# Optimization experiments

Measured on AMD Instinct MI355X. Metric: run time of the kernel, lower is better.

Reference implementation:

```python
import jax, jax.numpy as jnp
import numpy as np

D_MODEL = 256
D_STATE = 256
BATCH = 32
SEQ = 4096
RMIN, RMAX = 0.9, 0.999
NEG_SLOPE = 0.01
EPS = 1e-5


def layer_norm(x, w=None, b=None):
    m = jnp.mean(x, axis=-1, keepdims=True)
    v = jnp.var(x, axis=-1, keepdims=True)
    y = (x - m) * jax.lax.rsqrt(v + EPS)
    if w is not None:
        y = y * w + b
    return y


def leaky_relu(x):
    return jnp.where(x >= 0, x, NEG_SLOPE * x)


def setup_inputs() -> dict:
    key = jax.random.key(0)
    ks = jax.random.split(key, 12)
    x = jax.random.normal(ks[0], (BATCH, SEQ, D_MODEL), dtype=jnp.float32)
    # LRU ring init: |lambda| uniform in [rmin, rmax], phase uniform in [0, 2pi]
    u1 = jax.random.uniform(ks[1], (D_STATE,), dtype=jnp.float32)
    u2 = jax.random.uniform(ks[2], (D_STATE,), dtype=jnp.float32)
    nu_log = jnp.log(-0.5 * jnp.log(u1 * (RMAX**2 - RMIN**2) + RMIN**2))
    theta_log = jnp.log(2 * jnp.pi * u2)
    lam_mod = jnp.exp(-jnp.exp(nu_log))
    gamma_log = jnp.log(jnp.sqrt(1.0 - lam_mod**2))
    B_re = jax.random.normal(ks[3], (D_STATE, D_MODEL)) / np.sqrt(2 * D_MODEL)
    B_im = jax.random.normal(ks[4], (D_STATE, D_MODEL)) / np.sqrt(2 * D_MODEL)
    C_re = jax.random.normal(ks[5], (D_STATE, D_STATE)) / np.sqrt(D_STATE)
    C_im = jax.random.normal(ks[6], (D_STATE, D_STATE)) / np.sqrt(D_STATE)
    Dm = jax.random.normal(ks[7], (D_STATE, D_MODEL)) / np.sqrt(D_MODEL)
    Wl = jax.random.normal(ks[8], (D_MODEL, D_STATE)) / np.sqrt(D_STATE)
    bl = jax.random.normal(ks[9], (D_MODEL,)) * 0.02
    Wr = jax.random.normal(ks[10], (D_MODEL, D_STATE)) / np.sqrt(D_STATE)
    br = jax.random.normal(ks[11], (D_MODEL,)) * 0.02
    ones_m = jnp.ones((D_MODEL,), jnp.float32)
    zeros_m = jnp.zeros((D_MODEL,), jnp.float32)
    ones_s = jnp.ones((D_STATE,), jnp.float32)
    zeros_s = jnp.zeros((D_STATE,), jnp.float32)
    return {
        "x": x,
        "ln1_w": ones_m, "ln1_b": zeros_m,
        "nu_log": nu_log, "theta_log": theta_log, "gamma_log": gamma_log,
        "B_re": B_re, "B_im": B_im, "C_re": C_re, "C_im": C_im, "Dm": Dm,
        "ln2_w": ones_s, "ln2_b": zeros_s,
        "Wl": Wl, "bl": bl, "Wr": Wr, "br": br,
        "ln4_w": ones_m, "ln4_b": zeros_m,
    }


def reference(x, ln1_w, ln1_b, nu_log, theta_log, gamma_log, B_re, B_im,
              C_re, C_im, Dm, ln2_w, ln2_b, Wl, bl, Wr, br, ln4_w, ln4_b):
    # pre-norm + residual skip
    x1 = layer_norm(x, ln1_w, ln1_b)          # [B, T, d_model]
    skip = x1
    u = leaky_relu(x1)
    # LRU: h_t = lambda * h_{t-1} + gamma * (B u_t); y = Re(C h) + D u
    lam_mod = jnp.exp(-jnp.exp(nu_log))
    theta = jnp.exp(theta_log)
    lr = lam_mod * jnp.cos(theta)             # [N]
    li = lam_mod * jnp.sin(theta)
    gam = jnp.exp(gamma_log)
    bu_re = gam * jnp.einsum('btd,nd->btn', u, B_re)  # [B, T, N]
    bu_im = gam * jnp.einsum('btd,nd->btn', u, B_im)
    bu_re_t = jnp.swapaxes(bu_re, 0, 1)       # [T, B, N]
    bu_im_t = jnp.swapaxes(bu_im, 0, 1)

    def step(carry, inp):
        hr, hi = carry
        br_t, bi_t = inp
        hr2 = lr * hr - li * hi + br_t
        hi2 = lr * hi + li * hr + bi_t
        return (hr2, hi2), (hr2, hi2)

    h0 = (jnp.zeros((x.shape[0], lr.shape[0]), x.dtype),
          jnp.zeros((x.shape[0], lr.shape[0]), x.dtype))
    (hr_last, hi_last), (hr, hi) = jax.lax.scan(step, h0, (bu_re_t, bu_im_t))
    hr = jnp.swapaxes(hr, 0, 1)               # [B, T, N]
    hi = jnp.swapaxes(hi, 0, 1)
    y = (jnp.einsum('btn,mn->btm', hr, C_re)
         - jnp.einsum('btn,mn->btm', hi, C_im)
         + jnp.einsum('btd,md->btm', u, Dm))  # [B, T, d_state]
    # post-norm + nonlinearity
    y = leaky_relu(layer_norm(y, ln2_w, ln2_b))
    # gated bilinear MLP
    xl = layer_norm(y @ Wl.T + bl)            # no affine
    xr = layer_norm(y @ Wr.T + br)
    out = layer_norm(xl * xr, ln4_w, ln4_b) + skip
    return out
```

## Files before the change

### kernel.cpp

```cpp
#include <hip/hip_runtime.h>
#include <cstdint>
#include <cstddef>

#define DEV __device__ __forceinline__

typedef unsigned short u16;
typedef short short8 __attribute__((ext_vector_type(8)));
typedef float floatx4 __attribute__((ext_vector_type(4)));

constexpr int BB = 32;
constexpr int TT = 4096;
constexpr int RR = BB * TT;
constexpr int CH = 64;
constexpr int LC = TT / CH;

constexpr size_t OFF_LAM  = 0;
constexpr size_t OFF_LAML = 2048;
constexpr size_t OFF_GAM  = 4096;
constexpr size_t OFF_B1   = 8192;
constexpr size_t OFF_B2   = OFF_B1 + (size_t)512 * 256 * 2;
constexpr size_t OFF_B3   = OFF_B2 + (size_t)256 * 768 * 2;
constexpr size_t OFF_BIG  = 2ull << 20;
constexpr size_t SZB      = (size_t)RR * 256 * 2;

DEV float bf2f(u16 u) {
    unsigned int i = ((unsigned int)u) << 16;
    float f;
    __builtin_memcpy(&f, &i, 4);
    return f;
}
DEV u16 f2bf(float f) {
    unsigned int i;
    __builtin_memcpy(&i, &f, 4);
    i += 0x7fffu + ((i >> 16) & 1u);
    return (u16)(i >> 16);
}

DEV void gload16(const void* g, void* l) {
    __builtin_amdgcn_global_load_lds(
        (const __attribute__((address_space(1))) unsigned int*)g,
        (__attribute__((address_space(3))) unsigned int*)l, 16, 0, 0);
}
DEV void gload4(const void* g, void* l) {
    __builtin_amdgcn_global_load_lds(
        (const __attribute__((address_space(1))) unsigned int*)g,
        (__attribute__((address_space(3))) unsigned int*)l, 4, 0, 0);
}

__global__ __launch_bounds__(256)
void k_setup(const float* __restrict__ nu_log, const float* __restrict__ theta_log,
             const float* __restrict__ gamma_log,
             const float* __restrict__ B_re, const float* __restrict__ B_im,
             const float* __restrict__ C_re, const float* __restrict__ C_im,
             const float* __restrict__ Dm,
             const float* __restrict__ Wl, const float* __restrict__ Wr,
             char* __restrict__ ws)
{
    float2* lam  = (float2*)(ws + OFF_LAM);
    float2* lamL = (float2*)(ws + OFF_LAML);
    float*  gam  = (float*)(ws + OFF_GAM);
    u16* B1 = (u16*)(ws + OFF_B1);
    u16* B2 = (u16*)(ws + OFF_B2);
    u16* B3 = (u16*)(ws + OFF_B3);
    int g = blockIdx.x * 256 + threadIdx.x;
    int stride = gridDim.x * 256;
    if (g < 256) {
        float mod = expf(-expf(nu_log[g]));
        float th  = expf(theta_log[g]);
        float lr = mod * cosf(th), li = mod * sinf(th);
        lam[g] = make_float2(lr, li);
        gam[g] = expf(gamma_log[g]);
        float pr = 1.f, pi = 0.f;
        for (int i = 0; i < LC; i++) { float nr = pr*lr - pi*li; pi = pr*li + pi*lr; pr = nr; }
        lamL[g] = make_float2(pr, pi);
    }
    for (int i = g; i < 512*256; i += stride) {
        int n = i >> 8, d = i & 255;
        B1[i] = f2bf(n < 256 ? B_re[n*256 + d] : B_im[(n-256)*256 + d]);
    }
    for (int i = g; i < 256*768; i += stride) {
        int m = i / 768, k = i - m*768;
        float v = (k < 256) ? C_re[m*256 + k]
                : (k < 512) ? -C_im[m*256 + (k-256)]
                            : Dm[m*256 + (k-512)];
        B2[i] = f2bf(v);
    }
    for (int i = g; i < 512*256; i += stride) {
        int n = i >> 8, d = i & 255;
        B3[i] = f2bf(n < 256 ? Wl[n*256 + d] : Wr[(n-256)*256 + d]);
    }
}

__global__ __launch_bounds__(256)
void k_ln1(const float* __restrict__ x, const float* __restrict__ w, const float* __restrict__ b,
           u16* __restrict__ u, u16* __restrict__ skip)
{
    const int wv = threadIdx.x >> 6, lane = threadIdx.x & 63;
    const size_t row = (size_t)blockIdx.x * 4 + wv;
    float4 v = ((const float4*)(x + row * 256))[lane];
    float s = v.x + v.y + v.z + v.w;
    float q = v.x*v.x + v.y*v.y + v.z*v.z + v.w*v.w;
    #pragma unroll
    for (int o = 32; o; o >>= 1) { s += __shfl_xor(s, o); q += __shfl_xor(q, o); }
    const float m  = s * (1.f/256.f);
    const float rs = rsqrtf(q * (1.f/256.f) - m*m + 1e-5f);
    const float4 wv4 = ((const float4*)w)[lane];
    const float4 bv4 = ((const float4*)b)[lane];
    float y0 = (v.x - m) * rs * wv4.x + bv4.x;
    float y1 = (v.y - m) * rs * wv4.y + bv4.y;
    float y2 = (v.z - m) * rs * wv4.z + bv4.z;
    float y3 = (v.w - m) * rs * wv4.w + bv4.w;
    ((ushort4*)(skip + row * 256))[lane] = make_ushort4(f2bf(y0), f2bf(y1), f2bf(y2), f2bf(y3));
    float u0 = y0 >= 0.f ? y0 : 0.01f * y0;
    float u1 = y1 >= 0.f ? y1 : 0.01f * y1;
    float u2 = y2 >= 0.f ? y2 : 0.01f * y2;
    float u3 = y3 >= 0.f ? y3 : 0.01f * y3;
    ((ushort4*)(u + row * 256))[lane] = make_ushort4(f2bf(u0), f2bf(u1), f2bf(u2), f2bf(u3));
}

__global__ __launch_bounds__(256)
void k_gemm1(const u16* __restrict__ A0, const u16* __restrict__ Bmat,
             u16* __restrict__ O0, u16* __restrict__ O1, const float* __restrict__ p0)
{
    __shared__ alignas(16) u16 As[2][128 * 64];
    __shared__ alignas(16) u16 Bs[2][128 * 64];
    const int wid = threadIdx.x >> 6, lane = threadIdx.x & 63;
    const int rowbase = blockIdx.x * 128;
    const int ct = blockIdx.y;
    const u16* Bbase = Bmat + (size_t)ct * 128 * 256;
    const int srow  = lane >> 3;
    const int sslot = (lane & 7) ^ srow;
    floatx4 acc[4][4] = {};

    auto stage = [&](int kt, int pb) {
        int kofs = kt * 64;
        #pragma unroll
        for (int i = 0; i < 4; i++) {
            int grp = wid * 4 + i;
            int row = grp * 8 + srow;
            gload16(A0 + (size_t)(rowbase + row) * 256 + kofs + sslot * 8,
                    (char*)&As[pb][0] + grp * 1024);
            gload16(Bbase + (size_t)row * 256 + kofs + sslot * 8,
                    (char*)&Bs[pb][0] + grp * 1024);
        }
    };

    stage(0, 0);
    const int wm = wid >> 1, wn = wid & 1;
    for (int kt = 0; kt < 4; ++kt) {
        const int pb = kt & 1;
        if (kt + 1 < 4) {
            stage(kt + 1, pb ^ 1);
            asm volatile("s_waitcnt vmcnt(8)" ::: "memory");
        } else {
            asm volatile("s_waitcnt vmcnt(0)" ::: "memory");
        }
        __builtin_amdgcn_s_barrier();
        short8 af[2][4], bfr[2][4];
        #pragma unroll
        for (int kk = 0; kk < 2; kk++) {
            const int rslot = (kk * 4 + (lane >> 4)) ^ (lane & 7);
            #pragma unroll
            for (int mi = 0; mi < 4; mi++)
                af[kk][mi] = *(const short8*)&As[pb][(wm*64 + mi*16 + (lane & 15)) * 64 + rslot * 8];
            #pragma unroll
            for (int ni = 0; ni < 4; ni++)
                bfr[kk][ni] = *(const short8*)&Bs[pb][(wn*64 + ni*16 + (lane & 15)) * 64 + rslot * 8];
        }
        #pragma unroll
        for (int mi = 0; mi < 4; mi++)
            #pragma unroll
            for (int ni = 0; ni < 4; ni++) {
                acc[mi][ni] = __builtin_amdgcn_mfma_f32_16x16x32_bf16(af[0][mi], bfr[0][ni], acc[mi][ni], 0, 0, 0);
                acc[mi][ni] = __builtin_amdgcn_mfma_f32_16x16x32_bf16(af[1][mi], bfr[1][ni], acc[mi][ni], 0, 0, 0);
            }
        __builtin_amdgcn_s_barrier();
    }
    #pragma unroll
    for (int mi = 0; mi < 4; mi++) {
        #pragma unroll
        for (int ni = 0; ni < 4; ni++) {
            const int cc = wn*64 + ni*16 + (lane & 15);
            const int n  = ct * 128 + cc;
            u16* outp = (n < 256) ? O0 : O1;
            const int col = n & 255;
            const float scale = p0[col];
            #pragma unroll
            for (int r = 0; r < 4; r++) {
                const int row = rowbase + wm*64 + mi*16 + ((lane >> 4) << 2) + r;
                outp[(size_t)row * 256 + col] = f2bf(acc[mi][ni][r] * scale);
            }
        }
    }
}

__global__ __launch_bounds__(512)
void k_gemm2(const u16* __restrict__ Ahr, const u16* __restrict__ Ahi, const u16* __restrict__ Au,
             const u16* __restrict__ Bm, u16* __restrict__ Oy,
             const float* __restrict__ w2, const float* __restrict__ b2)
{
    __shared__ alignas(16) char smem[49152 + 4096];
    u16*   As0 = (u16*)smem;
    u16*   Bs0 = (u16*)(smem + 16384);
    float* st  = (float*)(smem + 49152);
    const int tid = threadIdx.x, wid = tid >> 6, lane = tid & 63;
    const int lanelo = lane & 15, lanehi = lane >> 4;
    const int rowbase = blockIdx.x * 128;
    const int wm = wid >> 2, wn = wid & 3;
    floatx4 acc[4][4] = {};

    auto stage = [&](int kt, int pb) {
        const u16* Asrc = (kt < 8) ? Ahr : (kt < 16) ? Ahi : Au;
        const int kofs = (kt & 7) * 32;
        { int g = tid; int row = g >> 2, slot = g & 3;
          gload16(Asrc + (size_t)(rowbase + row) * 256 + kofs + slot * 8,
                  (char*)(As0 + pb * 4096) + (wid * 64) * 16); }
        #pragma unroll
        for (int j = 0; j < 2; j++) {
            int g = j * 512 + tid; int row = g >> 2, slot = g & 3;
            gload16(Bm + (size_t)row * 768 + kt * 32 + slot * 8,
                    (char*)(Bs0 + pb * 8192) + (j * 512 + wid * 64) * 16);
        }
    };

    stage(0, 0);
    for (int kt = 0; kt < 24; ++kt) {
        const int pb = kt & 1;
        if (kt + 1 < 24) {
            stage(kt + 1, pb ^ 1);
            asm volatile("s_waitcnt vmcnt(3)" ::: "memory");
        } else {
            asm volatile("s_waitcnt vmcnt(0)" ::: "memory");
        }
        __builtin_amdgcn_s_barrier();
        short8 af[4], bfr[4];
        #pragma unroll
        for (int mi = 0; mi < 4; mi++)
            af[mi] = *(const short8*)&As0[pb*4096 + (wm*64 + mi*16 + lanelo)*32 + lanehi*8];
        #pragma unroll
        for (int ni = 0; ni < 4; ni++)
            bfr[ni] = *(const short8*)&Bs0[pb*8192 + (wn*64 + ni*16 + lanelo)*32 + lanehi*8];
        #pragma unroll
        for (int mi = 0; mi < 4; mi++)
            #pragma unroll
            for (int ni = 0; ni < 4; ni++)
                acc[mi][ni] = __builtin_amdgcn_mfma_f32_16x16x32_bf16(af[mi], bfr[ni], acc[mi][ni], 0, 0, 0);
        __builtin_amdgcn_s_barrier();
    }

    float sarr[4][4], qarr[4][4];
    #pragma unroll
    for (int mi = 0; mi < 4; mi++)
        #pragma unroll
        for (int r = 0; r < 4; r++) {
            float s = 0.f, q = 0.f;
            #pragma unroll
            for (int ni = 0; ni < 4; ni++) { float v = acc[mi][ni][r]; s += v; q += v*v; }
            sarr[mi][r] = s; qarr[mi][r] = q;
        }
    #pragma unroll
    for (int o = 1; o < 16; o <<= 1)
        #pragma unroll
        for (int mi = 0; mi < 4; mi++)
            #pragma unroll
            for (int r = 0; r < 4; r++) {
                sarr[mi][r] += __shfl_xor(sarr[mi][r], o);
                qarr[mi][r] += __shfl_xor(qarr[mi][r], o);
            }
    if (lanelo == 0) {
        #pragma unroll
        for (int mi = 0; mi < 4; mi++)
            #pragma unroll
            for (int r = 0; r < 4; r++) {
                int rw = mi*16 + lanehi*4 + r;
                st[(wid*64 + rw)*2 + 0] = sarr[mi][r];
                st[(wid*64 + rw)*2 + 1] = qarr[mi][r];
            }
    }
    __syncthreads();
    float wc[4], bc[4];
    #pragma unroll
    for (int ni = 0; ni < 4; ni++) {
        int col = wn*64 + ni*16 + lanelo;
        wc[ni] = w2[col]; bc[ni] = b2[col];
    }
    #pragma unroll
    for (int mi = 0; mi < 4; mi++)
        #pragma unroll
        for (int r = 0; r < 4; r++) {
            const int rw = mi*16 + lanehi*4 + r;
            float S = 0.f, Q = 0.f;
            #pragma unroll
            for (int ww = 0; ww < 4; ww++) {
                S += st[((wm*4 + ww)*64 + rw)*2 + 0];
                Q += st[((wm*4 + ww)*64 + rw)*2 + 1];
            }
            const float m  = S * (1.f/256.f);
            const float rs = rsqrtf(Q * (1.f/256.f) - m*m + 1e-5f);
            const size_t row = (size_t)rowbase + wm*64 + rw;
            #pragma unroll
            for (int ni = 0; ni < 4; ni++) {
                int col = wn*64 + ni*16 + lanelo;
                float v = (acc[mi][ni][r] - m) * rs * wc[ni] + bc[ni];
                v = v >= 0.f ? v : 0.01f * v;
                Oy[row * 256 + col] = f2bf(v);
            }
        }
}

__global__ __launch_bounds__(512)
void k_gemm3f(const u16* __restrict__ Ay, const u16* __restrict__ Bm,
              const float* __restrict__ bl, const float* __restrict__ brr,
              const float* __restrict__ w4, const float* __restrict__ b4,
              const u16* __restrict__ skip, float* __restrict__ out)
{
    __shared__ alignas(16) char smem[73728];
    u16*   As0 = (u16*)smem;
    u16*   Bs0 = (u16*)(smem + 8192);
    float* xrb = (float*)smem;
    float* st  = (float*)(smem + 65536);
    float* st4 = (float*)(smem + 65536 + 4096);
    const int tid = threadIdx.x, wid = tid >> 6, lane = tid & 63;
    const int lanelo = lane & 15, lanehi = lane >> 4;
    const int rowbase = blockIdx.x * 64;
    const int wn = wid;
    floatx4 acc[4][4] = {};

    auto stage = [&](int kt, int pb) {
        const int kofs = kt * 32;
        #pragma unroll
        for (int j = 0; j < 2; j++) {
            int d = j * 512 + tid; int row = d >> 4, dc = d & 15;
            gload4(Ay + (size_t)(rowbase + row) * 256 + kofs + dc * 2,
                   (char*)(As0 + pb * 2048) + (j * 512 + wid * 64) * 4);
        }
        #pragma unroll
        for (int j = 0; j < 4; j++) {
            int g = j * 512 + tid; int row = g >> 2, slot = g & 3;
            gload16(Bm + (size_t)row * 256 + kofs + slot * 8,
                    (char*)(Bs0 + pb * 16384) + (j * 512 + wid * 64) * 16);
        }
    };

    stage(0, 0);
    for (int kt = 0; kt < 8; ++kt) {
        const int pb = kt & 1;
        if (kt + 1 < 8) {
            stage(kt + 1, pb ^ 1);
            asm volatile("s_waitcnt vmcnt(6)" ::: "memory");
        } else {
            asm volatile("s_waitcnt vmcnt(0)" ::: "memory");
        }
        __builtin_amdgcn_s_barrier();
        short8 af[4], bfr[4];
        #pragma unroll
        for (int mi = 0; mi < 4; mi++)
            af[mi] = *(const short8*)&As0[pb*2048 + (mi*16 + lanelo)*32 + lanehi*8];
        #pragma unroll
        for (int ni = 0; ni < 4; ni++)
            bfr[ni] = *(const short8*)&Bs0[pb*16384 + (wn*64 + ni*16 + lanelo)*32 + lanehi*8];
        #pragma unroll
        for (int mi = 0; mi < 4; mi++)
            #pragma unroll
            for (int ni = 0; ni < 4; ni++)
                acc[mi][ni] = __builtin_amdgcn_mfma_f32_16x16x32_bf16(af[mi], bfr[ni], acc[mi][ni], 0, 0, 0);
        __builtin_amdgcn_s_barrier();
    }

    float bc[4];
    #pragma unroll
    for (int ni = 0; ni < 4; ni++) {
        int col = wn*64 + ni*16 + lanelo;
        bc[ni] = (col < 256) ? bl[col] : brr[col - 256];
    }
    #pragma unroll
    for (int mi = 0; mi < 4; mi++)
        #pragma unroll
        for (int ni = 0; ni < 4; ni++)
            #pragma unroll
            for (int r = 0; r < 4; r++)
                acc[mi][ni][r] += bc[ni];
    float sarr[4][4], qarr[4][4];
    #pragma unroll
    for (int mi = 0; mi < 4; mi++)
        #pragma unroll
        for (int r = 0; r < 4; r++) {
            float s = 0.f, q = 0.f;
            #pragma unroll
            for (int ni = 0; ni < 4; ni++) { float v = acc[mi][ni][r]; s += v; q += v*v; }
            sarr[mi][r] = s; qarr[mi][r] = q;
        }
    #pragma unroll
    for (int o = 1; o < 16; o <<= 1)
        #pragma unroll
        for (int mi = 0; mi < 4; mi++)
            #pragma unroll
            for (int r = 0; r < 4; r++) {
                sarr[mi][r] += __shfl_xor(sarr[mi][r], o);
                qarr[mi][r] += __shfl_xor(qarr[mi][r], o);
            }
    __syncthreads();
    if (lanelo == 0) {
        #pragma unroll
        for (int mi = 0; mi < 4; mi++)
            #pragma unroll
            for (int r = 0; r < 4; r++) {
                int rw = mi*16 + lanehi*4 + r;
                st[(wid*64 + rw)*2 + 0] = sarr[mi][r];
                st[(wid*64 + rw)*2 + 1] = qarr[mi][r];
            }
    }
    __syncthreads();
    const int half = wn >> 2;
    #pragma unroll
    for (int mi = 0; mi < 4; mi++)
        #pragma unroll
        for (int r = 0; r < 4; r++) {
            const int rw = mi*16 + lanehi*4 + r;
            float S = 0.f, Q = 0.f;
            #pragma unroll
            for (int ww = 0; ww < 4; ww++) {
                S += st[((half*4 + ww)*64 + rw)*2 + 0];
                Q += st[((half*4 + ww)*64 + rw)*2 + 1];
            }
            const float m  = S * (1.f/256.f);
            const float rs = rsqrtf(Q * (1.f/256.f) - m*m + 1e-5f);
            #pragma unroll
            for (int ni = 0; ni < 4; ni++)
                acc[mi][ni][r] = (acc[mi][ni][r] - m) * rs;
        }
    if (half) {
        #pragma unroll
        for (int mi = 0; mi < 4; mi++)
            #pragma unroll
            for (int r = 0; r < 4; r++) {
                const int rw = mi*16 + lanehi*4 + r;
                #pragma unroll
                for (int ni = 0; ni < 4; ni++)
                    xrb[rw*256 + (wn - 4)*64 + ni*16 + lanelo] = acc[mi][ni][r];
            }
    }
    __syncthreads();
    if (!half) {
        #pragma unroll
        for (int mi = 0; mi < 4; mi++)
            #pragma unroll
            for (int r = 0; r < 4; r++) {
                const int rw = mi*16 + lanehi*4 + r;
                float s = 0.f, q = 0.f;
                #pragma unroll
                for (int ni = 0; ni < 4; ni++) {
                    float p = acc[mi][ni][r] * xrb[rw*256 + wn*64 + ni*16 + lanelo];
                    acc[mi][ni][r] = p;
                    s += p; q += p*p;
                }
                sarr[mi][r] = s; qarr[mi][r] = q;
            }
        #pragma unroll
        for (int o = 1; o < 16; o <<= 1)
            #pragma unroll
            for (int mi = 0; mi < 4; mi++)
                #pragma unroll
                for (int r = 0; r < 4; r++) {
                    sarr[mi][r] += __shfl_xor(sarr[mi][r], o);
                    qarr[mi][r] += __shfl_xor(qarr[mi][r], o);
                }
        if (lanelo == 0) {
            #pragma unroll
            for (int mi = 0; mi < 4; mi++)
                #pragma unroll
                for (int r = 0; r < 4; r++) {
                    int rw = mi*16 + lanehi*4 + r;
                    st4[(wn*64 + rw)*2 + 0] = sarr[mi][r];
                    st4[(wn*64 + rw)*2 + 1] = qarr[mi][r];
                }
        }
    }
    __syncthreads();
    if (!half) {
        float w4c[4], b4c[4];
        #pragma unroll
        for (int ni = 0; ni < 4; ni++) {
            int col = wn*64 + ni*16 + lanelo;
            w4c[ni] = w4[col]; b4c[ni] = b4[col];
        }
        #pragma unroll
        for (int mi = 0; mi < 4; mi++)
            #pragma unroll
            for (int r = 0; r < 4; r++) {
                const int rw = mi*16 + lanehi*4 + r;
                float S = 0.f, Q = 0.f;
                #pragma unroll
                for (int ww = 0; ww < 4; ww++) {
                    S += st4[(ww*64 + rw)*2 + 0];
                    Q += st4[(ww*64 + rw)*2 + 1];
                }
                const float m  = S * (1.f/256.f);
                const float rs = rsqrtf(Q * (1.f/256.f) - m*m + 1e-5f);
                const size_t row = (size_t)rowbase + rw;
                #pragma unroll
                for (int ni = 0; ni < 4; ni++) {
                    int col = wn*64 + ni*16 + lanelo;
                    float o = (acc[mi][ni][r] - m) * rs * w4c[ni] + b4c[ni]
                            + bf2f(skip[row*256 + col]);
                    out[row*256 + col] = o;
                }
            }
    }
}

__global__ __launch_bounds__(128)
void k_scan1(const u16* __restrict__ bre, const u16* __restrict__ bim,
             float4* __restrict__ carry, const char* __restrict__ ws)
{
    const float2* lam = (const float2*)(ws + OFF_LAM);
    const int b = blockIdx.x, c = blockIdx.y, p = threadIdx.x;
    const unsigned int* pre = (const unsigned int*)bre;
    const unsigned int* pim = (const unsigned int*)bim;
    const float2 l0 = lam[2*p], l1 = lam[2*p + 1];
    float hr0 = 0, hi0 = 0, hr1 = 0, hi1 = 0;
    size_t base = ((size_t)b * TT + (size_t)c * LC) * 128 + p;
    #pragma unroll 8
    for (int j = 0; j < LC; j++) {
        unsigned int re = pre[base + (size_t)j * 128];
        unsigned int im = pim[base + (size_t)j * 128];
        float br0 = bf2f((u16)(re & 0xffff)), br1 = bf2f((u16)(re >> 16));
        float bi0 = bf2f((u16)(im & 0xffff)), bi1 = bf2f((u16)(im >> 16));
        float nr0 = fmaf(l0.x, hr0, fmaf(-l0.y, hi0, br0));
        float ni0 = fmaf(l0.x, hi0, fmaf( l0.y, hr0, bi0));
        float nr1 = fmaf(l1.x, hr1, fmaf(-l1.y, hi1, br1));
        float ni1 = fmaf(l1.x, hi1, fmaf( l1.y, hr1, bi1));
        hr0 = nr0; hi0 = ni0; hr1 = nr1; hi1 = ni1;
    }
    carry[((size_t)b * CH + c) * 128 + p] = make_float4(hr0, hi0, hr1, hi1);
}

__global__ __launch_bounds__(128)
void k_comb(float4* __restrict__ carry, const char* __restrict__ ws)
{
    const float2* lamL = (const float2*)(ws + OFF_LAML);
    const int b = blockIdx.x, p = threadIdx.x;
    const float2 L0 = lamL[2*p], L1 = lamL[2*p + 1];
    float4 prev = make_float4(0.f, 0.f, 0.f, 0.f);
    size_t base = (size_t)b * CH * 128 + p;
    float4 nxt = carry[base];
    for (int c = 0; c < CH; c++) {
        float4 cur = nxt;
        if (c + 1 < CH) nxt = carry[base + (size_t)(c + 1) * 128];
        carry[base + (size_t)c * 128] = prev;
        float nx = fmaf(L0.x, prev.x, fmaf(-L0.y, prev.y, cur.x));
        float ny = fmaf(L0.x, prev.y, fmaf( L0.y, prev.x, cur.y));
        float nz = fmaf(L1.x, prev.z, fmaf(-L1.y, prev.w, cur.z));
        float nw = fmaf(L1.x, prev.w, fmaf( L1.y, prev.z, cur.w));
        prev = make_float4(nx, ny, nz, nw);
    }
}

__global__ __launch_bounds__(128)
void k_scan2(u16* __restrict__ bre, u16* __restrict__ bim,
             const float4* __restrict__ carry, const char* __restrict__ ws)
{
    const float2* lam = (const float2*)(ws + OFF_LAM);
    const int b = blockIdx.x, c = blockIdx.y, p = threadIdx.x;
    unsigned int* pre = (unsigned int*)bre;
    unsigned int* pim = (unsigned int*)bim;
    const float2 l0 = lam[2*p], l1 = lam[2*p + 1];
    float4 h0 = carry[((size_t)b * CH + c) * 128 + p];
    float hr0 = h0.x, hi0 = h0.y, hr1 = h0.z, hi1 = h0.w;
    size_t base = ((size_t)b * TT + (size_t)c * LC) * 128 + p;
    #pragma unroll 8
    for (int j = 0; j < LC; j++) {
        size_t idx = base + (size_t)j * 128;
        unsigned int re = pre[idx];
        unsigned int im = pim[idx];
        float br0 = bf2f((u16)(re & 0xffff)), br1 = bf2f((u16)(re >> 16));
        float bi0 = bf2f((u16)(im & 0xffff)), bi1 = bf2f((u16)(im >> 16));
        float nr0 = fmaf(l0.x, hr0, fmaf(-l0.y, hi0, br0));
        float ni0 = fmaf(l0.x, hi0, fmaf( l0.y, hr0, bi0));
        float nr1 = fmaf(l1.x, hr1, fmaf(-l1.y, hi1, br1));
        float ni1 = fmaf(l1.x, hi1, fmaf( l1.y, hr1, bi1));
        hr0 = nr0; hi0 = ni0; hr1 = nr1; hi1 = ni1;
        pre[idx] = ((unsigned int)f2bf(hr1) << 16) | f2bf(hr0);
        pim[idx] = ((unsigned int)f2bf(hi1) << 16) | f2bf(hi0);
    }
}

extern "C" void kernel_launch(void* const* d_in, const int* in_sizes, int n_in,
                              void* d_out, int out_size, void* d_ws, size_t ws_size,
                              hipStream_t stream)
{
    (void)in_sizes; (void)n_in; (void)out_size; (void)ws_size;
    const float* x         = (const float*)d_in[0];
    const float* ln1_w     = (const float*)d_in[1];
    const float* ln1_b     = (const float*)d_in[2];
    const float* nu_log    = (const float*)d_in[3];
    const float* theta_log = (const float*)d_in[4];
    const float* gamma_log = (const float*)d_in[5];
    const float* B_re      = (const float*)d_in[6];
    const float* B_im      = (const float*)d_in[7];
    const float* C_re      = (const float*)d_in[8];
    const float* C_im      = (const float*)d_in[9];
    const float* Dm        = (const float*)d_in[10];
    const float* ln2_w     = (const float*)d_in[11];
    const float* ln2_b     = (const float*)d_in[12];
    const float* Wl        = (const float*)d_in[13];
    const float* bl        = (const float*)d_in[14];
    const float* Wr        = (const float*)d_in[15];
    const float* br        = (const float*)d_in[16];
    const float* ln4_w     = (const float*)d_in[17];
    const float* ln4_b     = (const float*)d_in[18];

    char* ws = (char*)d_ws;
    float* gam = (float*)(ws + OFF_GAM);
    u16* B1 = (u16*)(ws + OFF_B1);
    u16* B2 = (u16*)(ws + OFF_B2);
    u16* B3 = (u16*)(ws + OFF_B3);
    u16* u    = (u16*)(ws + OFF_BIG);
    u16* skip = (u16*)(ws + OFF_BIG + 1 * SZB);
    u16* bure = (u16*)(ws + OFF_BIG + 2 * SZB);
    u16* buim = (u16*)(ws + OFF_BIG + 3 * SZB);
    u16* y    = (u16*)(ws + OFF_BIG + 4 * SZB);
    float4* carry = (float4*)(ws + OFF_BIG + 5 * SZB);
    float* out = (float*)d_out;

    k_setup<<<dim3(256), dim3(256), 0, stream>>>(nu_log, theta_log, gamma_log,
                                                 B_re, B_im, C_re, C_im, Dm, Wl, Wr, ws);
    k_ln1<<<dim3(RR/4), dim3(256), 0, stream>>>(x, ln1_w, ln1_b, u, skip);
    k_gemm1<<<dim3(RR/128, 4), dim3(256), 0, stream>>>(u, B1, bure, buim, gam);
    k_scan1<<<dim3(BB, CH), dim3(128), 0, stream>>>(bure, buim, carry, ws);
    k_comb<<<dim3(BB), dim3(128), 0, stream>>>(carry, ws);
    k_scan2<<<dim3(BB, CH), dim3(128), 0, stream>>>(bure, buim, carry, ws);
    k_gemm2<<<dim3(RR/128), dim3(512), 0, stream>>>(bure, buim, u, B2, y, ln2_w, ln2_b);
    k_gemm3f<<<dim3(RR/64), dim3(512), 0, stream>>>(y, B3, bl, br, ln4_w, ln4_b, skip, out);
}
```

Baseline: 477.8 us.

## Retile gated MLP GEMM to 128-row blocks with paired left/right columns per wave

```diff
diff --git a/kernel.cpp b/kernel.cpp
--- a/kernel.cpp
+++ b/kernel.cpp
@@ -40,11 +40,6 @@
     __builtin_amdgcn_global_load_lds(
         (const __attribute__((address_space(1))) unsigned int*)g,
         (__attribute__((address_space(3))) unsigned int*)l, 16, 0, 0);
-}
-DEV void gload4(const void* g, void* l) {
-    __builtin_amdgcn_global_load_lds(
-        (const __attribute__((address_space(1))) unsigned int*)g,
-        (__attribute__((address_space(3))) unsigned int*)l, 4, 0, 0);
 }
 
 __global__ __launch_bounds__(256)
@@ -308,37 +303,35 @@
         }
 }
 
-__global__ __launch_bounds__(512)
+__global__ __launch_bounds__(1024)
 void k_gemm3f(const u16* __restrict__ Ay, const u16* __restrict__ Bm,
               const float* __restrict__ bl, const float* __restrict__ brr,
               const float* __restrict__ w4, const float* __restrict__ b4,
               const u16* __restrict__ skip, float* __restrict__ out)
 {
-    __shared__ alignas(16) char smem[73728];
+    __shared__ alignas(16) char smem[81920];
     u16*   As0 = (u16*)smem;
-    u16*   Bs0 = (u16*)(smem + 8192);
-    float* xrb = (float*)smem;
-    float* st  = (float*)(smem + 65536);
-    float* st4 = (float*)(smem + 65536 + 4096);
+    u16*   Bs0 = (u16*)(smem + 16384);
+    float* st  = (float*)smem;
+    float* st4 = (float*)(smem + 16384);
     const int tid = threadIdx.x, wid = tid >> 6, lane = tid & 63;
     const int lanelo = lane & 15, lanehi = lane >> 4;
-    const int rowbase = blockIdx.x * 64;
-    const int wn = wid;
+    const int rowbase = blockIdx.x * 128;
+    const int wm = wid >> 3, wn = wid & 7;
     floatx4 acc[4][4] = {};
 
     auto stage = [&](int kt, int pb) {
         const int kofs = kt * 32;
+        if (tid < 512) {
+            int row = tid >> 2, slot = tid & 3;
+            gload16(Ay + (size_t)(rowbase + row) * 256 + kofs + slot * 8,
+                    (char*)(As0 + pb * 4096) + wid * 1024);
+        }
         #pragma unroll
         for (int j = 0; j < 2; j++) {
-            int d = j * 512 + tid; int row = d >> 4, dc = d & 15;
-            gload4(Ay + (size_t)(rowbase + row) * 256 + kofs + dc * 2,
-                   (char*)(As0 + pb * 2048) + (j * 512 + wid * 64) * 4);
-        }
-        #pragma unroll
-        for (int j = 0; j < 4; j++) {
-            int g = j * 512 + tid; int row = g >> 2, slot = g & 3;
+            int g = j * 1024 + tid; int row = g >> 2, slot = g & 3;
             gload16(Bm + (size_t)row * 256 + kofs + slot * 8,
-                    (char*)(Bs0 + pb * 16384) + (j * 512 + wid * 64) * 16);
+                    (char*)(Bs0 + pb * 16384) + (j * 1024 + wid * 64) * 16);
         }
     };
 
@@ -347,7 +340,8 @@
         const int pb = kt & 1;
         if (kt + 1 < 8) {
             stage(kt + 1, pb ^ 1);
-            asm volatile("s_waitcnt vmcnt(6)" ::: "memory");
+            if (wid < 8) asm volatile("s_waitcnt vmcnt(3)" ::: "memory");
+            else         asm volatile("s_waitcnt vmcnt(2)" ::: "memory");
         } else {
             asm volatile("s_waitcnt vmcnt(0)" ::: "memory");
         }
@@ -355,10 +349,12 @@
         short8 af[4], bfr[4];
         #pragma unroll
         for (int mi = 0; mi < 4; mi++)
-            af[mi] = *(const short8*)&As0[pb*2048 + (mi*16 + lanelo)*32 + lanehi*8];
-        #pragma unroll
-        for (int ni = 0; ni < 4; ni++)
-            bfr[ni] = *(const short8*)&Bs0[pb*16384 + (wn*64 + ni*16 + lanelo)*32 + lanehi*8];
+            af[mi] = *(const short8*)&As0[pb*4096 + (wm*64 + mi*16 + lanelo)*32 + lanehi*8];
+        #pragma unroll
+        for (int ni = 0; ni < 4; ni++) {
+            const int s = wn*32 + (ni&1)*16 + (ni>>1)*256 + lanelo;
+            bfr[ni] = *(const short8*)&Bs0[pb*16384 + s*32 + lanehi*8];
+        }
         #pragma unroll
         for (int mi = 0; mi < 4; mi++)
             #pragma unroll
@@ -366,147 +362,98 @@
                 acc[mi][ni] = __builtin_amdgcn_mfma_f32_16x16x32_bf16(af[mi], bfr[ni], acc[mi][ni], 0, 0, 0);
         __builtin_amdgcn_s_barrier();
     }
-
-    float bc[4];
-    #pragma unroll
-    for (int ni = 0; ni < 4; ni++) {
-        int col = wn*64 + ni*16 + lanelo;
-        bc[ni] = (col < 256) ? bl[col] : brr[col - 256];
+    __syncthreads();
+
+    float bcl[2], bcr[2];
+    #pragma unroll
+    for (int j = 0; j < 2; j++) {
+        const int cl = wn*32 + j*16 + lanelo;
+        bcl[j] = bl[cl]; bcr[j] = brr[cl];
     }
     #pragma unroll
     for (int mi = 0; mi < 4; mi++)
         #pragma unroll
-        for (int ni = 0; ni < 4; ni++)
-            #pragma unroll
-            for (int r = 0; r < 4; r++)
-                acc[mi][ni][r] += bc[ni];
-    float sarr[4][4], qarr[4][4];
+        for (int r = 0; r < 4; r++) {
+            acc[mi][0][r] += bcl[0]; acc[mi][1][r] += bcl[1];
+            acc[mi][2][r] += bcr[0]; acc[mi][3][r] += bcr[1];
+        }
     #pragma unroll
     for (int mi = 0; mi < 4; mi++)
         #pragma unroll
         for (int r = 0; r < 4; r++) {
-            float s = 0.f, q = 0.f;
-            #pragma unroll
-            for (int ni = 0; ni < 4; ni++) { float v = acc[mi][ni][r]; s += v; q += v*v; }
-            sarr[mi][r] = s; qarr[mi][r] = q;
-        }
-    #pragma unroll
-    for (int o = 1; o < 16; o <<= 1)
-        #pragma unroll
-        for (int mi = 0; mi < 4; mi++)
-            #pragma unroll
-            for (int r = 0; r < 4; r++) {
-                sarr[mi][r] += __shfl_xor(sarr[mi][r], o);
-                qarr[mi][r] += __shfl_xor(qarr[mi][r], o);
-            }
+            float a0 = acc[mi][0][r], a1 = acc[mi][1][r];
+            float b0 = acc[mi][2][r], b1 = acc[mi][3][r];
+            float sLv = a0 + a1, qLv = a0*a0 + a1*a1;
+            float sRv = b0 + b1, qRv = b0*b0 + b1*b1;
+            #pragma unroll
+            for (int o = 1; o < 16; o <<= 1) {
+                sLv += __shfl_xor(sLv, o); qLv += __shfl_xor(qLv, o);
+                sRv += __shfl_xor(sRv, o); qRv += __shfl_xor(qRv, o);
+            }
+            if (lanelo == 0) {
+                const int rw = mi*16 + lanehi*4 + r;
+                float* p = &st[(wid*64 + rw)*4];
+                p[0] = sLv; p[1] = qLv; p[2] = sRv; p[3] = qRv;
+            }
+        }
     __syncthreads();
-    if (lanelo == 0) {
-        #pragma unroll
-        for (int mi = 0; mi < 4; mi++)
-            #pragma unroll
-            for (int r = 0; r < 4; r++) {
-                int rw = mi*16 + lanehi*4 + r;
-                st[(wid*64 + rw)*2 + 0] = sarr[mi][r];
-                st[(wid*64 + rw)*2 + 1] = qarr[mi][r];
-            }
-    }
-    __syncthreads();
-    const int half = wn >> 2;
     #pragma unroll
     for (int mi = 0; mi < 4; mi++)
         #pragma unroll
         for (int r = 0; r < 4; r++) {
             const int rw = mi*16 + lanehi*4 + r;
-            float S = 0.f, Q = 0.f;
-            #pragma unroll
-            for (int ww = 0; ww < 4; ww++) {
-                S += st[((half*4 + ww)*64 + rw)*2 + 0];
-                Q += st[((half*4 + ww)*64 + rw)*2 + 1];
-            }
-            const float m  = S * (1.f/256.f);
-            const float rs = rsqrtf(Q * (1.f/256.f) - m*m + 1e-5f);
-            #pragma unroll
-            for (int ni = 0; ni < 4; ni++)
-                acc[mi][ni][r] = (acc[mi][ni][r] - m) * rs;
-        }
-    if (half) {
-        #pragma unroll
-        for (int mi = 0; mi < 4; mi++)
-            #pragma unroll
-            for (int r = 0; r < 4; r++) {
-                const int rw = mi*16 + lanehi*4 + r;
-                #pragma unroll
-                for (int ni = 0; ni < 4; ni++)
-                    xrb[rw*256 + (wn - 4)*64 + ni*16 + lanelo] = acc[mi][ni][r];
-            }
-    }
+            float SL = 0.f, QL = 0.f, SR = 0.f, QR = 0.f;
+            #pragma unroll
+            for (int ww = 0; ww < 8; ww++) {
+                const float* p = &st[((wm*8 + ww)*64 + rw)*4];
+                SL += p[0]; QL += p[1]; SR += p[2]; QR += p[3];
+            }
+            const float mL = SL * (1.f/256.f);
+            const float rsL = rsqrtf(QL * (1.f/256.f) - mL*mL + 1e-5f);
+            const float mR = SR * (1.f/256.f);
+            const float rsR = rsqrtf(QR * (1.f/256.f) - mR*mR + 1e-5f);
+            float p0 = ((acc[mi][0][r] - mL) * rsL) * ((acc[mi][2][r] - mR) * rsR);
+            float p1 = ((acc[mi][1][r] - mL) * rsL) * ((acc[mi][3][r] - mR) * rsR);
+            acc[mi][0][r] = p0; acc[mi][1][r] = p1;
+            float s4 = p0 + p1, q4 = p0*p0 + p1*p1;
+            #pragma unroll
+            for (int o = 1; o < 16; o <<= 1) {
+                s4 += __shfl_xor(s4, o); q4 += __shfl_xor(q4, o);
+            }
+            if (lanelo == 0) {
+                float* p = &st4[(wid*64 + rw)*2];
+                p[0] = s4; p[1] = q4;
+            }
+        }
     __syncthreads();
-    if (!half) {
-        #pragma unroll
-        for (int mi = 0; mi < 4; mi++)
-            #pragma unroll
-            for (int r = 0; r < 4; r++) {
-                const int rw = mi*16 + lanehi*4 + r;
-                float s = 0.f, q = 0.f;
-                #pragma unroll
-                for (int ni = 0; ni < 4; ni++) {
-                    float p = acc[mi][ni][r] * xrb[rw*256 + wn*64 + ni*16 + lanelo];
-                    acc[mi][ni][r] = p;
-                    s += p; q += p*p;
-                }
-                sarr[mi][r] = s; qarr[mi][r] = q;
-            }
-        #pragma unroll
-        for (int o = 1; o < 16; o <<= 1)
-            #pragma unroll
-            for (int mi = 0; mi < 4; mi++)
-                #pragma unroll
-                for (int r = 0; r < 4; r++) {
-                    sarr[mi][r] += __shfl_xor(sarr[mi][r], o);
-                    qarr[mi][r] += __shfl_xor(qarr[mi][r], o);
-                }
-        if (lanelo == 0) {
-            #pragma unroll
-            for (int mi = 0; mi < 4; mi++)
-                #pragma unroll
-                for (int r = 0; r < 4; r++) {
-                    int rw = mi*16 + lanehi*4 + r;
-                    st4[(wn*64 + rw)*2 + 0] = sarr[mi][r];
-                    st4[(wn*64 + rw)*2 + 1] = qarr[mi][r];
-                }
-        }
-    }
-    __syncthreads();
-    if (!half) {
-        float w4c[4], b4c[4];
-        #pragma unroll
-        for (int ni = 0; ni < 4; ni++) {
-            int col = wn*64 + ni*16 + lanelo;
-            w4c[ni] = w4[col]; b4c[ni] = b4[col];
-        }
-        #pragma unroll
-        for (int mi = 0; mi < 4; mi++)
-            #pragma unroll
-            for (int r = 0; r < 4; r++) {
-                const int rw = mi*16 + lanehi*4 + r;
-                float S = 0.f, Q = 0.f;
-                #pragma unroll
-                for (int ww = 0; ww < 4; ww++) {
-                    S += st4[(ww*64 + rw)*2 + 0];
-                    Q += st4[(ww*64 + rw)*2 + 1];
-                }
-                const float m  = S * (1.f/256.f);
-                const float rs = rsqrtf(Q * (1.f/256.f) - m*m + 1e-5f);
-                const size_t row = (size_t)rowbase + rw;
-                #pragma unroll
-                for (int ni = 0; ni < 4; ni++) {
-                    int col = wn*64 + ni*16 + lanelo;
-                    float o = (acc[mi][ni][r] - m) * rs * w4c[ni] + b4c[ni]
-                            + bf2f(skip[row*256 + col]);
-                    out[row*256 + col] = o;
-                }
-            }
-    }
+    float w4c[2], b4c[2];
+    #pragma unroll
+    for (int j = 0; j < 2; j++) {
+        const int col = wn*32 + j*16 + lanelo;
+        w4c[j] = w4[col]; b4c[j] = b4[col];
+    }
+    #pragma unroll
+    for (int mi = 0; mi < 4; mi++)
+        #pragma unroll
+        for (int r = 0; r < 4; r++) {
+            const int rw = mi*16 + lanehi*4 + r;
+            float S4 = 0.f, Q4 = 0.f;
+            #pragma unroll
+            for (int ww = 0; ww < 8; ww++) {
+                const float* p = &st4[((wm*8 + ww)*64 + rw)*2];
+                S4 += p[0]; Q4 += p[1];
+            }
+            const float m4 = S4 * (1.f/256.f);
+            const float rs4 = rsqrtf(Q4 * (1.f/256.f) - m4*m4 + 1e-5f);
+            const size_t row = (size_t)rowbase + wm*64 + rw;
+            #pragma unroll
+            for (int j = 0; j < 2; j++) {
+                const int col = wn*32 + j*16 + lanelo;
+                float o = (acc[mi][j][r] - m4) * rs4 * w4c[j] + b4c[j]
+                        + bf2f(skip[row*256 + col]);
+                out[row*256 + col] = o;
+            }
+        }
 }
 
 __global__ __launch_bounds__(128)
@@ -631,5 +578,5 @@
     k_comb<<<dim3(BB), dim3(128), 0, stream>>>(carry, ws);
     k_scan2<<<dim3(BB, CH), dim3(128), 0, stream>>>(bure, buim, carry, ws);
     k_gemm2<<<dim3(RR/128), dim3(512), 0, stream>>>(bure, buim, u, B2, y, ln2_w, ln2_b);
-    k_gemm3f<<<dim3(RR/64), dim3(512), 0, stream>>>(y, B3, bl, br, ln4_w, ln4_b, skip, out);
-}
+    k_gemm3f<<<dim3(RR/128), dim3(1024), 0, stream>>>(y, B3, bl, br, ln4_w, ln4_b, skip, out);
+}
```

Measured after the change: 479.6 us. Within noise of the previous version (+0.4%).
